# Kernel tuning notes

Hardware: AMD Instinct MI355X
Metric: run time of the kernel (lower is better)

Reference implementation:

```python
import jax, jax.numpy as jnp
import numpy as np

N_HEAD = 16
MEMORY = 256  # band width: key j visible to query i iff i-MEMORY <= j <= i


def setup_inputs() -> dict:
    key = jax.random.key(0)
    k1, k2, k3 = jax.random.split(key, 3)
    B, T, C = 2, 2048, 1024
    x = jax.random.normal(k1, (B, T, C), dtype=jnp.float32)
    # Linear weights stored in x @ W layout (equivalent to torch Linear with W^T)
    W_attn = jax.random.normal(k2, (C, 3 * C), dtype=jnp.float32) * (1.0 / np.sqrt(C))
    W_proj = jax.random.normal(k3, (C, C), dtype=jnp.float32) * (1.0 / np.sqrt(C))
    return {"x": x, "W_attn": W_attn, "W_proj": W_proj}


def reference(x, W_attn, W_proj):
    B, T, C = x.shape
    H = N_HEAD
    D = C // H
    qkv = x @ W_attn                                   # [B,T,3C]
    q, k, v = jnp.split(qkv, 3, axis=-1)
    # [B,T,C] -> [B,H,T,D]
    q = q.reshape(B, T, H, D).transpose(0, 2, 1, 3)
    k = k.reshape(B, T, H, D).transpose(0, 2, 1, 3)
    v = v.reshape(B, T, H, D).transpose(0, 2, 1, 3)
    scale = 1.0 / np.sqrt(D)
    scores = jnp.einsum('bhqd,bhkd->bhqk', q, k) * scale
    # banded causal mask: j <= i and j >= i - MEMORY
    i = jnp.arange(T)[:, None]
    j = jnp.arange(T)[None, :]
    mask = (j <= i) & (j >= i - MEMORY)                # [T,T] bool
    scores = jnp.where(mask[None, None], scores, -jnp.inf)
    att = jax.nn.softmax(scores, axis=-1)              # each row has >=1 valid entry
    y = jnp.einsum('bhqk,bhkd->bhqd', att, v)          # [B,H,T,D]
    y = y.transpose(0, 2, 1, 3).reshape(B, T, C)
    return y @ W_proj
```

## Files before the change

kernel.cpp:

```cpp
#include <hip/hip_runtime.h>

typedef __bf16 bf16;
typedef __bf16 bf16x4 __attribute__((ext_vector_type(4)));
typedef __bf16 bf16x8 __attribute__((ext_vector_type(8)));
typedef float f32x4 __attribute__((ext_vector_type(4)));

#define T_SEQ 2048
#define CDIM  1024
#define QKV_LD 3072
#define MEM   256

#define GLOAD_LDS16(gp, lp) __builtin_amdgcn_global_load_lds( \
    (const __attribute__((address_space(1))) unsigned int*)(gp), \
    (__attribute__((address_space(3))) unsigned int*)(lp), 16, 0, 0)

#define BAR() do { __builtin_amdgcn_s_barrier(); asm volatile("" ::: "memory"); } while (0)

__global__ __launch_bounds__(256) void cast_f32_bf16_kernel(const float* __restrict__ in,
                                                            bf16* __restrict__ out, int n4) {
    int i = blockIdx.x * 256 + threadIdx.x;
    if (i < n4) {
        float4 v = reinterpret_cast<const float4*>(in)[i];
        bf16x4 o = { (bf16)v.x, (bf16)v.y, (bf16)v.z, (bf16)v.w };
        reinterpret_cast<bf16x4*>(out)[i] = o;
    }
}

__global__ __launch_bounds__(256) void transpose_cast_kernel(const float* __restrict__ W,
                                                             bf16* __restrict__ Wt,
                                                             int K, int N) {
    __shared__ float tile[64][65];
    const int n0 = blockIdx.x * 64;
    const int k0 = blockIdx.y * 64;
    const int t  = threadIdx.x;
    const int tr = t >> 4;
    const int tc = (t & 15) * 4;
#pragma unroll
    for (int it = 0; it < 4; ++it) {
        int r = it * 16 + tr;
        float4 v = *reinterpret_cast<const float4*>(&W[(size_t)(k0 + r) * N + n0 + tc]);
        tile[r][tc + 0] = v.x; tile[r][tc + 1] = v.y;
        tile[r][tc + 2] = v.z; tile[r][tc + 3] = v.w;
    }
    __syncthreads();
#pragma unroll
    for (int it = 0; it < 4; ++it) {
        int n = it * 16 + tr;
        bf16x4 o;
#pragma unroll
        for (int j = 0; j < 4; ++j) o[j] = (bf16)tile[tc + j][n];
        *reinterpret_cast<bf16x4*>(&Wt[(size_t)(n0 + n) * K + k0 + tc]) = o;
    }
}

__global__ __launch_bounds__(256) void transpose_v_kernel(const bf16* __restrict__ qkv,
                                                          bf16* __restrict__ Vt) {
    const int bid = blockIdx.x;
    const int tt = bid & 31, h = (bid >> 5) & 15, b = bid >> 9;
    __shared__ bf16 tile[64][72];
    const int i = threadIdx.x;
    {
        const int tr = i >> 2, dc = (i & 3) * 16;
        const bf16* src = qkv + (size_t)(b * T_SEQ + tt * 64 + tr) * QKV_LD + 2 * CDIM + h * 64 + dc;
        *reinterpret_cast<bf16x8*>(&tile[tr][dc])     = *reinterpret_cast<const bf16x8*>(src);
        *reinterpret_cast<bf16x8*>(&tile[tr][dc + 8]) = *reinterpret_cast<const bf16x8*>(src + 8);
    }
    __syncthreads();
    {
        const int dr = i >> 2, tc = (i & 3) * 16;
        bf16x8 o0, o1;
#pragma unroll
        for (int j = 0; j < 8; ++j) { o0[j] = tile[tc + j][dr]; o1[j] = tile[tc + 8 + j][dr]; }
        bf16* dst = Vt + ((size_t)((b * 16 + h) * 64 + dr)) * T_SEQ + tt * 64 + tc;
        *reinterpret_cast<bf16x8*>(dst)     = o0;
        *reinterpret_cast<bf16x8*>(dst + 8) = o1;
    }
}

__global__ __launch_bounds__(512, 1) void gemm256_kernel(const bf16* __restrict__ A,
                                                         const bf16* __restrict__ Bt,
                                                         bf16* __restrict__ Cb,
                                                         int M, int N, int K) {
    __shared__ bf16 smA[2][256][64];
    __shared__ bf16 smB[2][192][64];
    const int t    = threadIdx.x;
    const int lane = t & 63;
    const int w    = t >> 6;
    const int wm   = (w >> 2) * 128;
    const int wn   = (w & 3) * 48;
    const int g    = lane >> 4;
    const int r    = lane & 15;

    const int nwg = gridDim.x, cpx = nwg >> 3;
    const int swz = (blockIdx.x & 7) * cpx + (blockIdx.x >> 3);
    const int ntn = N / 192;
    const int m0 = (swz / ntn) * 256;
    const int n0 = (swz % ntn) * 192;

    const bf16* Ab = A  + (size_t)m0 * K;
    const bf16* Bb = Bt + (size_t)n0 * K;
    const int NT = K >> 6;

#define STAGE_A(bi, u, kt) do { \
        const bf16* _s = Ab + (size_t)((u) * 64 + w * 8 + (lane >> 3)) * K \
                         + (kt) * 64 + ((lane & 7) ^ (lane >> 3)) * 8; \
        GLOAD_LDS16(_s, &smA[bi][(u) * 64 + w * 8][0]); \
    } while (0)
#define STAGE_B(bi, u, kt) do { \
        const bf16* _s = Bb + (size_t)((u) * 64 + w * 8 + (lane >> 3)) * K \
                         + (kt) * 64 + ((lane & 7) ^ (lane >> 3)) * 8; \
        GLOAD_LDS16(_s, &smB[bi][(u) * 64 + w * 8][0]); \
    } while (0)

    const int ch0 = ((g     ) ^ (r & 7)) * 8;
    const int ch1 = ((g ^ 4) ^ (r & 7)) * 8;

    const f32x4 zero4 = {0.f, 0.f, 0.f, 0.f};
    f32x4 acc[8][3];
#pragma unroll
    for (int i = 0; i < 8; ++i)
#pragma unroll
        for (int j = 0; j < 3; ++j) acc[i][j] = zero4;

    bf16x8 afr0[4][2], afr1[4][2], bfrA[2][2], bfrB[1][2];

#define MGRP(AF, FMB, BF, FNB, NF) do { \
    __builtin_amdgcn_s_setprio(1); \
    _Pragma("unroll") \
    for (int fm2 = 0; fm2 < 4; ++fm2) \
    _Pragma("unroll") \
    for (int fn2 = 0; fn2 < (NF); ++fn2) \
    _Pragma("unroll") \
    for (int kh = 0; kh < 2; ++kh) \
        acc[(FMB)+fm2][(FNB)+fn2] = __builtin_amdgcn_mfma_f32_16x16x32_bf16( \
            AF[fm2][kh], BF[fn2][kh], acc[(FMB)+fm2][(FNB)+fn2], 0, 0, 0); \
    __builtin_amdgcn_s_setprio(0); } while (0)

    STAGE_A(0, 0, 0); STAGE_A(0, 1, 0); STAGE_A(0, 2, 0); STAGE_A(0, 3, 0);
    STAGE_B(0, 0, 0); STAGE_B(0, 1, 0); STAGE_B(0, 2, 0);
    STAGE_A(1, 0, 1); STAGE_A(1, 1, 1); STAGE_A(1, 2, 1); STAGE_A(1, 3, 1);
    asm volatile("s_waitcnt vmcnt(4)" ::: "memory");
    __builtin_amdgcn_sched_barrier(0);
    BAR();

    for (int kt = 0; kt < NT; ++kt) {
        const int cur = kt & 1, nxt = cur ^ 1;
#pragma unroll
        for (int i = 0; i < 4; ++i) {
            afr0[i][0] = *reinterpret_cast<const bf16x8*>(&smA[cur][wm + i * 16 + r][ch0]);
            afr0[i][1] = *reinterpret_cast<const bf16x8*>(&smA[cur][wm + i * 16 + r][ch1]);
        }
#pragma unroll
        for (int fn = 0; fn < 2; ++fn) {
            bfrA[fn][0] = *reinterpret_cast<const bf16x8*>(&smB[cur][wn + fn * 16 + r][ch0]);
            bfrA[fn][1] = *reinterpret_cast<const bf16x8*>(&smB[cur][wn + fn * 16 + r][ch1]);
        }
#pragma unroll
        for (int i = 0; i < 4; ++i) {
            afr1[i][0] = *reinterpret_cast<const bf16x8*>(&smA[cur][wm + 64 + i * 16 + r][ch0]);
            afr1[i][1] = *reinterpret_cast<const bf16x8*>(&smA[cur][wm + 64 + i * 16 + r][ch1]);
        }
        bfrB[0][0] = *reinterpret_cast<const bf16x8*>(&smB[cur][wn + 32 + r][ch0]);
        bfrB[0][1] = *reinterpret_cast<const bf16x8*>(&smB[cur][wn + 32 + r][ch1]);
        if (kt + 1 < NT) { STAGE_B(nxt, 0, kt + 1); STAGE_B(nxt, 1, kt + 1); STAGE_B(nxt, 2, kt + 1); }
        __builtin_amdgcn_sched_barrier(0);
        BAR();

        MGRP(afr0, 0, bfrA, 0, 2);
        if (kt + 2 < NT) STAGE_A(cur, 0, kt + 2);
        MGRP(afr1, 4, bfrA, 0, 2);
        if (kt + 2 < NT) { STAGE_A(cur, 1, kt + 2); STAGE_A(cur, 2, kt + 2); }
        MGRP(afr1, 4, bfrB, 2, 1);
        if (kt + 2 < NT) STAGE_A(cur, 3, kt + 2);
        MGRP(afr0, 0, bfrB, 2, 1);

        if (kt >= NT - 2)      { asm volatile("s_waitcnt vmcnt(0)" ::: "memory"); }
        else                   { asm volatile("s_waitcnt vmcnt(4)" ::: "memory"); }
        __builtin_amdgcn_sched_barrier(0);
        BAR();
    }

#pragma unroll
    for (int fm = 0; fm < 8; ++fm)
#pragma unroll
        for (int fn = 0; fn < 3; ++fn)
#pragma unroll
            for (int e = 0; e < 4; ++e) {
                int row = m0 + wm + fm * 16 + g * 4 + e;
                int col = n0 + wn + fn * 16 + r;
                Cb[(size_t)row * N + col] = (bf16)acc[fm][fn][e];
            }
#undef STAGE_A
#undef STAGE_B
#undef MGRP
}

template<bool OUT_BF16>
__global__ __launch_bounds__(256) void gemm_bt_kernel(const bf16* __restrict__ A,
                                                      const bf16* __restrict__ Bt,
                                                      bf16* __restrict__ Cb,
                                                      float* __restrict__ Cf,
                                                      int M, int N, int K) {
    __shared__ bf16 As[128 * 32];
    __shared__ bf16 Bs[128 * 32];
    const int t    = threadIdx.x;
    const int lane = t & 63;
    const int w    = t >> 6;
    const int wm   = (w >> 1) * 64;
    const int wn   = (w & 1) * 64;
    const int g    = lane >> 4;
    const int r    = lane & 15;
    const int m0   = blockIdx.y * 128;
    const int n0   = blockIdx.x * 128;

    const bf16* Ab = A  + (size_t)m0 * K;
    const bf16* Bb = Bt + (size_t)n0 * K;
    const bf16* Ag0 = Ab + (size_t)(w * 32 + (lane >> 2)) * K + (lane & 3) * 8;
    const bf16* Ag1 = Ab + (size_t)(w * 32 + 16 + (lane >> 2)) * K + (lane & 3) * 8;
    const bf16* Bg0 = Bb + (size_t)(w * 32 + (lane >> 2)) * K + (lane & 3) * 8;
    const bf16* Bg1 = Bb + (size_t)(w * 32 + 16 + (lane >> 2)) * K + (lane & 3) * 8;

    bf16* ldsA0 = As + (w * 32) * 32;
    bf16* ldsA1 = As + (w * 32 + 16) * 32;
    bf16* ldsB0 = Bs + (w * 32) * 32;
    bf16* ldsB1 = Bs + (w * 32 + 16) * 32;

    const f32x4 zero4 = {0.f, 0.f, 0.f, 0.f};
    f32x4 acc[4][4];
#pragma unroll
    for (int i = 0; i < 4; ++i)
#pragma unroll
        for (int j = 0; j < 4; ++j) acc[i][j] = zero4;

    for (int k0 = 0; k0 < K; k0 += 32) {
        __syncthreads();
        GLOAD_LDS16(Ag0 + k0, ldsA0);
        GLOAD_LDS16(Ag1 + k0, ldsA1);
        GLOAD_LDS16(Bg0 + k0, ldsB0);
        GLOAD_LDS16(Bg1 + k0, ldsB1);
        __syncthreads();

        bf16x8 af[4], bfr[4];
#pragma unroll
        for (int i = 0; i < 4; ++i) {
            af[i]  = *reinterpret_cast<const bf16x8*>(&As[(wm + i * 16 + r) * 32 + g * 8]);
            bfr[i] = *reinterpret_cast<const bf16x8*>(&Bs[(wn + i * 16 + r) * 32 + g * 8]);
        }
#pragma unroll
        for (int i = 0; i < 4; ++i)
#pragma unroll
            for (int j = 0; j < 4; ++j)
                acc[i][j] = __builtin_amdgcn_mfma_f32_16x16x32_bf16(af[i], bfr[j], acc[i][j], 0, 0, 0);
    }

#pragma unroll
    for (int i = 0; i < 4; ++i)
#pragma unroll
        for (int j = 0; j < 4; ++j)
#pragma unroll
            for (int e = 0; e < 4; ++e) {
                int row = m0 + wm + i * 16 + g * 4 + e;
                int col = n0 + wn + j * 16 + r;
                if constexpr (OUT_BF16) Cb[(size_t)row * N + col] = (bf16)acc[i][j][e];
                else                    Cf[(size_t)row * N + col] = acc[i][j][e];
            }
}

__global__ __launch_bounds__(512) void attn_kernel(const bf16* __restrict__ qkv,
                                                   const bf16* __restrict__ Vt,
                                                   bf16* __restrict__ y) {
    __shared__ bf16 vtl[64 * 384];
    const int bid  = blockIdx.x;
    const int bh   = bid >> 4;
    const int qblk = bid & 15;
    const int b = bh >> 4, h = bh & 15;
    const int qb0 = qblk * 128;
    const int wlo = qb0 - 256;
    const int wv   = threadIdx.x >> 6;
    const int lane = threadIdx.x & 63;
    const int g = lane >> 4, c = lane & 15;
    const int q0 = qb0 + wv * 16;
    const int q = q0 + c;
    const float NEG_INF = -__builtin_inff();

    const bf16* base = qkv + (size_t)b * T_SEQ * QKV_LD;
    const bf16* Qb = base + h * 64;
    const bf16* Kb = base + CDIM + h * 64;
    const bf16* Vtb = Vt + (size_t)(b * 16 + h) * 64 * T_SEQ;

#pragma unroll
    for (int i = 0; i < 6; ++i) {
        const int Lb = (wv * 6 + i) * 1024 + lane * 16;
        const int d   = Lb / 768;
        const int c16 = (Lb % 768) >> 4;
        int koff = ((2 * c16) ^ (d & 14)) << 2;
        int gk = wlo + koff;
        gk = gk < 0 ? 0 : gk;
        GLOAD_LDS16(Vtb + (size_t)d * T_SEQ + gk, vtl + (wv * 6 + i) * 512);
    }

    const bf16x8 qf0 = *reinterpret_cast<const bf16x8*>(Qb + (size_t)q * QKV_LD + g * 8);
    const bf16x8 qf1 = *reinterpret_cast<const bf16x8*>(Qb + (size_t)q * QKV_LD + 32 + g * 8);

    __syncthreads();

    const f32x4 zero4 = {0.f, 0.f, 0.f, 0.f};
    f32x4 o[4];
#pragma unroll
    for (int cb = 0; cb < 4; ++cb) o[cb] = zero4;
    float m_run = NEG_INF, l_run = 0.f;

    const int jstart = (q0 - MEM > 0) ? (q0 - MEM) : 0;
    for (int j0 = jstart; j0 < q0 + 16; j0 += 32) {
        const int kr0 = j0 + c;
        int kr1 = j0 + 16 + c; kr1 = kr1 < T_SEQ ? kr1 : T_SEQ - 1;
        bf16x8 kf00 = *reinterpret_cast<const bf16x8*>(Kb + (size_t)kr0 * QKV_LD + g * 8);
        bf16x8 kf01 = *reinterpret_cast<const bf16x8*>(Kb + (size_t)kr0 * QKV_LD + 32 + g * 8);
        bf16x8 kf10 = *reinterpret_cast<const bf16x8*>(Kb + (size_t)kr1 * QKV_LD + g * 8);
        bf16x8 kf11 = *reinterpret_cast<const bf16x8*>(Kb + (size_t)kr1 * QKV_LD + 32 + g * 8);
        f32x4 s0 = __builtin_amdgcn_mfma_f32_16x16x32_bf16(kf00, qf0, zero4, 0, 0, 0);
        s0 = __builtin_amdgcn_mfma_f32_16x16x32_bf16(kf01, qf1, s0, 0, 0, 0);
        f32x4 s1 = __builtin_amdgcn_mfma_f32_16x16x32_bf16(kf10, qf0, zero4, 0, 0, 0);
        s1 = __builtin_amdgcn_mfma_f32_16x16x32_bf16(kf11, qf1, s1, 0, 0, 0);

        float mt = NEG_INF;
#pragma unroll
        for (int e = 0; e < 4; ++e) {
            int k0i = j0 + 4 * g + e;
            int k1i = k0i + 16;
            float v0 = (k0i <= q && k0i >= q - MEM) ? s0[e] * 0.125f : NEG_INF;
            float v1 = (k1i <= q && k1i >= q - MEM) ? s1[e] * 0.125f : NEG_INF;
            s0[e] = v0; s1[e] = v1;
            mt = fmaxf(mt, fmaxf(v0, v1));
        }
        mt = fmaxf(mt, __shfl_xor(mt, 16, 64));
        mt = fmaxf(mt, __shfl_xor(mt, 32, 64));
        const float mnew = fmaxf(m_run, mt);
        const float corr = __expf(m_run - mnew);

        float ps = 0.f;
        bf16x8 pav;
#pragma unroll
        for (int e = 0; e < 4; ++e) {
            float e0 = __expf(s0[e] - mnew);
            float e1 = __expf(s1[e] - mnew);
            ps += e0 + e1;
            pav[e]     = (bf16)e0;
            pav[4 + e] = (bf16)e1;
        }
        ps += __shfl_xor(ps, 16, 64);
        ps += __shfl_xor(ps, 32, 64);
        l_run = l_run * corr + ps;
        m_run = mnew;

#pragma unroll
        for (int cb = 0; cb < 4; ++cb) {
            o[cb][0] *= corr; o[cb][1] *= corr; o[cb][2] *= corr; o[cb][3] *= corr;
        }

        const int jrel = j0 - wlo;
        const int c8a = (jrel + 4 * g) >> 2;
        const int c8b = (c8a + 4 > 95) ? 95 : (c8a + 4);
#pragma unroll
        for (int cb = 0; cb < 4; ++cb) {
            const int d = cb * 16 + c;
            const int xx = d & 14;
            const bf16* vrow = vtl + d * 384;
            bf16x4 va  = *reinterpret_cast<const bf16x4*>(vrow + ((c8a ^ xx) << 2));
            bf16x4 vb2 = *reinterpret_cast<const bf16x4*>(vrow + ((c8b ^ xx) << 2));
            bf16x8 vf = { va[0], va[1], va[2], va[3], vb2[0], vb2[1], vb2[2], vb2[3] };
            o[cb] = __builtin_amdgcn_mfma_f32_16x16x32_bf16(vf, pav, o[cb], 0, 0, 0);
        }
    }

    const float linv = 1.0f / l_run;
    bf16* yr = y + (size_t)(b * T_SEQ + q) * CDIM + h * 64 + 4 * g;
#pragma unroll
    for (int cb = 0; cb < 4; ++cb) {
        bf16x4 ov = { (bf16)(o[cb][0] * linv), (bf16)(o[cb][1] * linv),
                      (bf16)(o[cb][2] * linv), (bf16)(o[cb][3] * linv) };
        *reinterpret_cast<bf16x4*>(yr + cb * 16) = ov;
    }
}

extern "C" void kernel_launch(void* const* d_in, const int* in_sizes, int n_in,
                              void* d_out, int out_size, void* d_ws, size_t ws_size,
                              hipStream_t stream) {
    const float* x      = (const float*)d_in[0];
    const float* W_attn = (const float*)d_in[1];
    const float* W_proj = (const float*)d_in[2];
    float* out = (float*)d_out;

    char* ws = (char*)d_ws;
    bf16* xb   = (bf16*)(ws);
    bf16* WaT  = (bf16*)(ws + 8388608);
    bf16* WpT  = (bf16*)(ws + 14680064);
    bf16* qkv  = (bf16*)(ws + 16777216);
    bf16* yatt = (bf16*)(ws + 41943040);
    bf16* Vt   = xb;

    cast_f32_bf16_kernel<<<4096, 256, 0, stream>>>(x, xb, 1048576);
    transpose_cast_kernel<<<dim3(48, 16), 256, 0, stream>>>(W_attn, WaT, 1024, 3072);
    transpose_cast_kernel<<<dim3(16, 16), 256, 0, stream>>>(W_proj, WpT, 1024, 1024);

    gemm256_kernel<<<256, 512, 0, stream>>>(xb, WaT, qkv, 4096, 3072, 1024);
    transpose_v_kernel<<<1024, 256, 0, stream>>>(qkv, Vt);
    attn_kernel<<<512, 512, 0, stream>>>(qkv, Vt, yatt);
    gemm_bt_kernel<false><<<dim3(8, 32), 256, 0, stream>>>(yatt, WpT, nullptr, out, 4096, 1024, 1024);
}
```

Baseline: 105.2 us.

## Fuse V transpose into QKV GEMM epilogue and prefetch K in attention

The QKV GEMM epilogue now writes the V columns straight into the transposed Vt layout, which removes the separate transpose_v kernel launch and its extra read and write of V. Vt gets its own workspace region because xb is still being read by the GEMM while it runs. The attention loop also loads the next K tile into registers before the current tile's MFMAs, to hide global load latency. The costs are more register pressure and scattered 8-byte stores to Vt in the epilogue.

```diff
diff --git a/kernel.cpp b/kernel.cpp
--- a/kernel.cpp
+++ b/kernel.cpp
@@ -53,33 +53,10 @@
     }
 }
 
-__global__ __launch_bounds__(256) void transpose_v_kernel(const bf16* __restrict__ qkv,
-                                                          bf16* __restrict__ Vt) {
-    const int bid = blockIdx.x;
-    const int tt = bid & 31, h = (bid >> 5) & 15, b = bid >> 9;
-    __shared__ bf16 tile[64][72];
-    const int i = threadIdx.x;
-    {
-        const int tr = i >> 2, dc = (i & 3) * 16;
-        const bf16* src = qkv + (size_t)(b * T_SEQ + tt * 64 + tr) * QKV_LD + 2 * CDIM + h * 64 + dc;
-        *reinterpret_cast<bf16x8*>(&tile[tr][dc])     = *reinterpret_cast<const bf16x8*>(src);
-        *reinterpret_cast<bf16x8*>(&tile[tr][dc + 8]) = *reinterpret_cast<const bf16x8*>(src + 8);
-    }
-    __syncthreads();
-    {
-        const int dr = i >> 2, tc = (i & 3) * 16;
-        bf16x8 o0, o1;
-#pragma unroll
-        for (int j = 0; j < 8; ++j) { o0[j] = tile[tc + j][dr]; o1[j] = tile[tc + 8 + j][dr]; }
-        bf16* dst = Vt + ((size_t)((b * 16 + h) * 64 + dr)) * T_SEQ + tt * 64 + tc;
-        *reinterpret_cast<bf16x8*>(dst)     = o0;
-        *reinterpret_cast<bf16x8*>(dst + 8) = o1;
-    }
-}
-
 __global__ __launch_bounds__(512, 1) void gemm256_kernel(const bf16* __restrict__ A,
                                                          const bf16* __restrict__ Bt,
                                                          bf16* __restrict__ Cb,
+                                                         bf16* __restrict__ Vt,
                                                          int M, int N, int K) {
     __shared__ bf16 smA[2][256][64];
     __shared__ bf16 smB[2][192][64];
@@ -183,13 +160,21 @@
 #pragma unroll
     for (int fm = 0; fm < 8; ++fm)
 #pragma unroll
-        for (int fn = 0; fn < 3; ++fn)
-#pragma unroll
-            for (int e = 0; e < 4; ++e) {
-                int row = m0 + wm + fm * 16 + g * 4 + e;
-                int col = n0 + wn + fn * 16 + r;
-                Cb[(size_t)row * N + col] = (bf16)acc[fm][fn][e];
+        for (int fn = 0; fn < 3; ++fn) {
+            const int col  = n0 + wn + fn * 16 + r;
+            const int row0 = m0 + wm + fm * 16 + g * 4;
+            if (col < 2 * CDIM) {
+#pragma unroll
+                for (int e = 0; e < 4; ++e)
+                    Cb[(size_t)(row0 + e) * N + col] = (bf16)acc[fm][fn][e];
+            } else {
+                const int hd = col - 2 * CDIM;
+                const int bb = row0 >> 11, tt = row0 & (T_SEQ - 1);
+                bf16x4 v = { (bf16)acc[fm][fn][0], (bf16)acc[fm][fn][1],
+                             (bf16)acc[fm][fn][2], (bf16)acc[fm][fn][3] };
+                *reinterpret_cast<bf16x4*>(&Vt[((size_t)(bb * 16 + (hd >> 6)) * 64 + (hd & 63)) * T_SEQ + tt]) = v;
             }
+        }
 #undef STAGE_A
 #undef STAGE_B
 #undef MGRP
@@ -310,18 +295,28 @@
     for (int cb = 0; cb < 4; ++cb) o[cb] = zero4;
     float m_run = NEG_INF, l_run = 0.f;
 
+#define LOAD_K(J0, K00, K01, K10, K11) do { \
+        const int _kr0 = (J0) + c; \
+        int _kr1 = (J0) + 16 + c; _kr1 = _kr1 < T_SEQ ? _kr1 : T_SEQ - 1; \
+        K00 = *reinterpret_cast<const bf16x8*>(Kb + (size_t)_kr0 * QKV_LD + g * 8); \
+        K01 = *reinterpret_cast<const bf16x8*>(Kb + (size_t)_kr0 * QKV_LD + 32 + g * 8); \
+        K10 = *reinterpret_cast<const bf16x8*>(Kb + (size_t)_kr1 * QKV_LD + g * 8); \
+        K11 = *reinterpret_cast<const bf16x8*>(Kb + (size_t)_kr1 * QKV_LD + 32 + g * 8); \
+    } while (0)
+
     const int jstart = (q0 - MEM > 0) ? (q0 - MEM) : 0;
+    bf16x8 kc00, kc01, kc10, kc11;
+    LOAD_K(jstart, kc00, kc01, kc10, kc11);
+
     for (int j0 = jstart; j0 < q0 + 16; j0 += 32) {
-        const int kr0 = j0 + c;
-        int kr1 = j0 + 16 + c; kr1 = kr1 < T_SEQ ? kr1 : T_SEQ - 1;
-        bf16x8 kf00 = *reinterpret_cast<const bf16x8*>(Kb + (size_t)kr0 * QKV_LD + g * 8);
-        bf16x8 kf01 = *reinterpret_cast<const bf16x8*>(Kb + (size_t)kr0 * QKV_LD + 32 + g * 8);
-        bf16x8 kf10 = *reinterpret_cast<const bf16x8*>(Kb + (size_t)kr1 * QKV_LD + g * 8);
-        bf16x8 kf11 = *reinterpret_cast<const bf16x8*>(Kb + (size_t)kr1 * QKV_LD + 32 + g * 8);
-        f32x4 s0 = __builtin_amdgcn_mfma_f32_16x16x32_bf16(kf00, qf0, zero4, 0, 0, 0);
-        s0 = __builtin_amdgcn_mfma_f32_16x16x32_bf16(kf01, qf1, s0, 0, 0, 0);
-        f32x4 s1 = __builtin_amdgcn_mfma_f32_16x16x32_bf16(kf10, qf0, zero4, 0, 0, 0);
-        s1 = __builtin_amdgcn_mfma_f32_16x16x32_bf16(kf11, qf1, s1, 0, 0, 0);
+        bf16x8 kn00, kn01, kn10, kn11;
+        const bool more = (j0 + 32 < q0 + 16);
+        if (more) LOAD_K(j0 + 32, kn00, kn01, kn10, kn11);
+
+        f32x4 s0 = __builtin_amdgcn_mfma_f32_16x16x32_bf16(kc00, qf0, zero4, 0, 0, 0);
+        s0 = __builtin_amdgcn_mfma_f32_16x16x32_bf16(kc01, qf1, s0, 0, 0, 0);
+        f32x4 s1 = __builtin_amdgcn_mfma_f32_16x16x32_bf16(kc10, qf0, zero4, 0, 0, 0);
+        s1 = __builtin_amdgcn_mfma_f32_16x16x32_bf16(kc11, qf1, s1, 0, 0, 0);
 
         float mt = NEG_INF;
 #pragma unroll
@@ -371,7 +366,10 @@
             bf16x8 vf = { va[0], va[1], va[2], va[3], vb2[0], vb2[1], vb2[2], vb2[3] };
             o[cb] = __builtin_amdgcn_mfma_f32_16x16x32_bf16(vf, pav, o[cb], 0, 0, 0);
         }
-    }
+
+        if (more) { kc00 = kn00; kc01 = kn01; kc10 = kn10; kc11 = kn11; }
+    }
+#undef LOAD_K
 
     const float linv = 1.0f / l_run;
     bf16* yr = y + (size_t)(b * T_SEQ + q) * CDIM + h * 64 + 4 * g;
@@ -397,14 +395,13 @@
     bf16* WpT  = (bf16*)(ws + 14680064);
     bf16* qkv  = (bf16*)(ws + 16777216);
     bf16* yatt = (bf16*)(ws + 41943040);
-    bf16* Vt   = xb;
+    bf16* Vt   = (bf16*)(ws + 50331648);
 
     cast_f32_bf16_kernel<<<4096, 256, 0, stream>>>(x, xb, 1048576);
     transpose_cast_kernel<<<dim3(48, 16), 256, 0, stream>>>(W_attn, WaT, 1024, 3072);
     transpose_cast_kernel<<<dim3(16, 16), 256, 0, stream>>>(W_proj, WpT, 1024, 1024);
 
-    gemm256_kernel<<<256, 512, 0, stream>>>(xb, WaT, qkv, 4096, 3072, 1024);
-    transpose_v_kernel<<<1024, 256, 0, stream>>>(qkv, Vt);
+    gemm256_kernel<<<256, 512, 0, stream>>>(xb, WaT, qkv, Vt, 4096, 3072, 1024);
     attn_kernel<<<512, 512, 0, stream>>>(qkv, Vt, yatt);
     gemm_bt_kernel<false><<<dim3(8, 32), 256, 0, stream>>>(yatt, WpT, nullptr, out, 4096, 1024, 1024);
 }
```

Measured after the change: 102.1 us. 1.03x faster.
